# Optimization experiments

Hardware: AMD Instinct MI355X
Metric: run time of the kernel (lower is better)

The kernel has to match this reference:

```python
import jax, jax.numpy as jnp
import numpy as np

S, B, C = 7, 2, 80
LAMBDA_COORDS = 5.0
LAMBDA_NOOBJ = 0.5


def _iou_cxcywh(a, b):
    """Elementwise IoU of boxes in cx,cy,w,h format, shapes (..., 4) -> (...).
    Same math as torchvision box_convert(cxcywh->xyxy) + box_iou diagonal,
    computed directly (O(S^2)) instead of the O(S^4) pairwise matrix."""
    ax1 = a[..., 0] - a[..., 2] * 0.5
    ay1 = a[..., 1] - a[..., 3] * 0.5
    ax2 = a[..., 0] + a[..., 2] * 0.5
    ay2 = a[..., 1] + a[..., 3] * 0.5
    bx1 = b[..., 0] - b[..., 2] * 0.5
    by1 = b[..., 1] - b[..., 3] * 0.5
    bx2 = b[..., 0] + b[..., 2] * 0.5
    by2 = b[..., 1] + b[..., 3] * 0.5
    inter_w = jnp.clip(jnp.minimum(ax2, bx2) - jnp.maximum(ax1, bx1), 0.0)
    inter_h = jnp.clip(jnp.minimum(ay2, by2) - jnp.maximum(ay1, by1), 0.0)
    inter = inter_w * inter_h
    area_a = (ax2 - ax1) * (ay2 - ay1)
    area_b = (bx2 - bx1) * (by2 - by1)
    return inter / (area_a + area_b - inter)


def setup_inputs() -> dict:
    key = jax.random.key(0)
    k1, k2 = jax.random.split(key)
    N = 8192
    predictions = jax.random.normal(k1, (N, S, S, C + 5 * B), dtype=jnp.float32)
    target = jax.random.uniform(k2, (N, S, S, C + 5), dtype=jnp.float32)
    return {"predictions": predictions, "target": target}


def reference(predictions, target):
    preds = predictions.reshape(-1, S, S, C + 5 * B)
    target_boxes = target[..., -4:]                 # (N,S,S,4)
    pred_boxes_1 = preds[..., -4:]
    pred_boxes_2 = preds[..., -9:-5]

    iou1 = _iou_cxcywh(pred_boxes_1, target_boxes)  # (N,S,S) == diag of box_iou
    iou2 = _iou_cxcywh(pred_boxes_2, target_boxes)
    ious_idx = jnp.argmax(jnp.stack([iou1, iou2], axis=0), axis=0)  # (N,S,S)

    m1 = (1 - ious_idx).astype(preds.dtype)  # responsible-box masks
    m2 = ious_idx.astype(preds.dtype)
    obj = target[..., -5]                    # objectness (N,S,S)

    pred_boxes = obj[..., None] * (m1[..., None] * pred_boxes_1 + m2[..., None] * pred_boxes_2)

    dims = jnp.sign(pred_boxes[..., -2:]) * jnp.sqrt(jnp.abs(pred_boxes[..., -2:]) + 1e-6)
    target_dims = jnp.sqrt(target_boxes[..., -2:])

    sse = lambda a, b: jnp.sum((a - b) ** 2)  # MSELoss(reduction='sum')

    center_loss = sse(pred_boxes[..., :-3], target_boxes[..., :-3]) * LAMBDA_COORDS
    dimensions_loss = sse(dims, target_dims) * LAMBDA_COORDS
    coords_loss = center_loss + dimensions_loss

    obj_pred = preds[..., -5] * m1 + preds[..., -10] * m2
    obj_loss = sse(obj * obj_pred, obj)
    noobj_loss = sse((1.0 - obj) * obj_pred, obj) * LAMBDA_NOOBJ

    classes_loss = sse(preds[..., :-10] * obj[..., None], target[..., :-5])

    return (coords_loss, obj_loss, noobj_loss, classes_loss)
```

## Files before the change

kernel.cpp:

```cpp
#include <hip/hip_runtime.h>


#define NPRED 90
#define NTGT  85
#define NCLS  80

__device__ __forceinline__ float sgnf(float x) {
    return (x > 0.0f) ? 1.0f : ((x < 0.0f) ? -1.0f : 0.0f);
}

__device__ __forceinline__ float iou_vs_target(
    float acx, float acy, float aw, float ah,
    float bx1, float by1, float bx2, float by2, float area_b)
{
    float ax1 = acx - aw * 0.5f, ay1 = acy - ah * 0.5f;
    float ax2 = acx + aw * 0.5f, ay2 = acy + ah * 0.5f;
    float iw = fmaxf(fminf(ax2, bx2) - fmaxf(ax1, bx1), 0.0f);
    float ih = fmaxf(fminf(ay2, by2) - fmaxf(ay1, by1), 0.0f);
    float inter = iw * ih;
    float area_a = (ax2 - ax1) * (ay2 - ay1);
    return inter / (area_a + area_b - inter);
}

__global__ __launch_bounds__(256) void yolo_loss_kernel(
    const float* __restrict__ preds, const float* __restrict__ targ,
    float* __restrict__ out, int n_cells)
{
    float coords = 0.0f, objl = 0.0f, noobjl = 0.0f, clsl = 0.0f;

    int tid    = blockIdx.x * 256 + threadIdx.x;
    int stride = gridDim.x * 256;

    for (int cell = tid; cell < n_cells; cell += stride) {
        const float* p = preds + (size_t)cell * NPRED;
        const float* t = targ  + (size_t)cell * NTGT;
        const float2* p2 = (const float2*)p;

        float obj = t[NCLS];

        float cls = 0.0f;
        #pragma unroll 10
        for (int k = 0; k < NCLS / 2; ++k) {
            float2 pv = p2[k];
            float d0 = fmaf(pv.x, obj, -t[2 * k]);
            float d1 = fmaf(pv.y, obj, -t[2 * k + 1]);
            cls = fmaf(d0, d0, cls);
            cls = fmaf(d1, d1, cls);
        }
        clsl += cls;

        float2 q0 = p2[40];
        float2 q1 = p2[41];
        float2 q2 = p2[42];
        float2 q3 = p2[43];
        float2 q4 = p2[44];

        float tcx = t[81], tcy = t[82], tw = t[83], th = t[84];
        float bx1 = tcx - tw * 0.5f, by1 = tcy - th * 0.5f;
        float bx2 = tcx + tw * 0.5f, by2 = tcy + th * 0.5f;
        float area_b = (bx2 - bx1) * (by2 - by1);

        float iou1 = iou_vs_target(q3.x, q3.y, q4.x, q4.y, bx1, by1, bx2, by2, area_b);
        float iou2 = iou_vs_target(q0.y, q1.x, q1.y, q2.x, bx1, by1, bx2, by2, area_b);
        bool use2 = iou2 > iou1;

        float pcx = obj * (use2 ? q0.y : q3.x);
        float pw  = obj * (use2 ? q1.y : q4.x);
        float ph  = obj * (use2 ? q2.x : q4.y);

        float dc = pcx - tcx;
        float dw = sgnf(pw) * sqrtf(fabsf(pw) + 1e-6f) - sqrtf(tw);
        float dh = sgnf(ph) * sqrtf(fabsf(ph) + 1e-6f) - sqrtf(th);
        coords = fmaf(dc, dc, coords);
        coords = fmaf(dw, dw, coords);
        coords = fmaf(dh, dh, coords);

        float obj_pred = use2 ? q0.x : q2.y;
        float e1 = fmaf(obj, obj_pred, -obj);
        objl = fmaf(e1, e1, objl);
        float e2 = fmaf(1.0f - obj, obj_pred, -obj);
        noobjl = fmaf(e2, e2, noobjl);
    }

    #pragma unroll
    for (int off = 32; off > 0; off >>= 1) {
        coords += __shfl_down(coords, off);
        objl   += __shfl_down(objl, off);
        noobjl += __shfl_down(noobjl, off);
        clsl   += __shfl_down(clsl, off);
    }

    __shared__ float red[4][4];
    int wave = threadIdx.x >> 6;
    int lane = threadIdx.x & 63;
    if (lane == 0) {
        red[0][wave] = coords;
        red[1][wave] = objl;
        red[2][wave] = noobjl;
        red[3][wave] = clsl;
    }
    __syncthreads();
    if (threadIdx.x == 0) {
        float c = red[0][0] + red[0][1] + red[0][2] + red[0][3];
        float o = red[1][0] + red[1][1] + red[1][2] + red[1][3];
        float n = red[2][0] + red[2][1] + red[2][2] + red[2][3];
        float k = red[3][0] + red[3][1] + red[3][2] + red[3][3];
        atomicAdd(&out[0], 5.0f * c);
        atomicAdd(&out[1], o);
        atomicAdd(&out[2], 0.5f * n);
        atomicAdd(&out[3], k);
    }
}

extern "C" void kernel_launch(void* const* d_in, const int* in_sizes, int n_in,
                              void* d_out, int out_size, void* d_ws, size_t ws_size,
                              hipStream_t stream) {
    const float* preds = (const float*)d_in[0];
    const float* targ  = (const float*)d_in[1];
    float* out = (float*)d_out;

    int n_cells = in_sizes[0] / NPRED;

    hipMemsetAsync(d_out, 0, (size_t)out_size * sizeof(float), stream);

    int blocks = (n_cells + 255) / 256;
    hipLaunchKernelGGL(yolo_loss_kernel, dim3(blocks), dim3(256), 0, stream,
                       preds, targ, out, n_cells);
}
```

Before: 333.3 us.

## Stage cell chunks through LDS with coalesced float4 loads

Instead of each thread reading one cell's 90+85 floats with strided accesses, each block loads a chunk of 64 cells with fully coalesced float4 loads, staging targets in shared memory and streaming prediction quads directly. Class loss is computed per quad with lookups into LDS targets, and box components are scattered to a small LDS buffer so 64 threads can compute the IoU and coordinate losses. This is meant to fix the uncoalesced per-thread strided global access pattern, at the cost of extra syncthreads, LDS traffic, per-element branching, and only a quarter of threads doing the box work.

```diff
diff --git a/kernel.cpp b/kernel.cpp
--- a/kernel.cpp
+++ b/kernel.cpp
@@ -4,6 +4,12 @@
 #define NPRED 90
 #define NTGT  85
 #define NCLS  80
+#define CHUNK 64
+#define TPB   256
+#define PBS   11
+
+#define NT4 (CHUNK * NTGT / 4)
+#define NP4 (CHUNK * NPRED / 4)
 
 __device__ __forceinline__ float sgnf(float x) {
     return (x > 0.0f) ? 1.0f : ((x < 0.0f) ? -1.0f : 0.0f);
@@ -22,60 +28,152 @@
     return inter / (area_a + area_b - inter);
 }
 
-__global__ __launch_bounds__(256) void yolo_loss_kernel(
+__device__ __forceinline__ void proc_elem(float v, int cl, int j,
+    const float* __restrict__ t_lds, float* __restrict__ pbox, float& clsl)
+{
+    if (j < NCLS) {
+        float obj = t_lds[cl * NTGT + NCLS];
+        float tv  = t_lds[cl * NTGT + j];
+        float d = fmaf(v, obj, -tv);
+        clsl = fmaf(d, d, clsl);
+    } else {
+        pbox[cl * PBS + (j - NCLS)] = v;
+    }
+}
+
+__device__ __forceinline__ void proc_quad(float4 v, int q,
+    const float* __restrict__ t_lds, float* __restrict__ pbox, float& clsl)
+{
+    int f  = 4 * q;
+    int cl = f / NPRED;
+    int j  = f - cl * NPRED;
+    proc_elem(v.x, cl, j, t_lds, pbox, clsl); ++j;
+    proc_elem(v.y, cl, j, t_lds, pbox, clsl); ++j;
+    if (j == NPRED) { j = 0; ++cl; }
+    proc_elem(v.z, cl, j, t_lds, pbox, clsl); ++j;
+    proc_elem(v.w, cl, j, t_lds, pbox, clsl);
+}
+
+__global__ __launch_bounds__(TPB) void yolo_loss_kernel(
     const float* __restrict__ preds, const float* __restrict__ targ,
     float* __restrict__ out, int n_cells)
 {
+    __shared__ __align__(16) float t_lds[CHUNK * NTGT];
+    __shared__ float pbox[CHUNK * PBS];
+    __shared__ float red[4][4];
+
     float coords = 0.0f, objl = 0.0f, noobjl = 0.0f, clsl = 0.0f;
 
-    int tid    = blockIdx.x * 256 + threadIdx.x;
-    int stride = gridDim.x * 256;
-
-    for (int cell = tid; cell < n_cells; cell += stride) {
+    const int tid = threadIdx.x;
+    const int n_chunks = n_cells / CHUNK;
+
+    for (int ch = blockIdx.x; ch < n_chunks; ch += gridDim.x) {
+        const float4* tg4 = (const float4*)(targ  + (size_t)ch * (CHUNK * NTGT));
+        const float4* pr4 = (const float4*)(preds + (size_t)ch * (CHUNK * NPRED));
+
+        float4 t0 = tg4[tid];
+        float4 t1 = tg4[tid + 256];
+        float4 t2 = tg4[tid + 512];
+        float4 t3 = tg4[tid + 768];
+        float4 t4 = tg4[tid + 1024];
+        const bool ht = tid < (NT4 - 1280);
+        float4 t5 = make_float4(0.f, 0.f, 0.f, 0.f);
+        if (ht) t5 = tg4[tid + 1280];
+
+        float4 p0 = pr4[tid];
+        float4 p1 = pr4[tid + 256];
+        float4 p2 = pr4[tid + 512];
+        float4 p3 = pr4[tid + 768];
+        float4 p4 = pr4[tid + 1024];
+        const bool hp = tid < (NP4 - 1280);
+        float4 p5 = make_float4(0.f, 0.f, 0.f, 0.f);
+        if (hp) p5 = pr4[tid + 1280];
+
+        __syncthreads();
+
+        float4* tl4 = (float4*)t_lds;
+        tl4[tid]        = t0;
+        tl4[tid + 256]  = t1;
+        tl4[tid + 512]  = t2;
+        tl4[tid + 768]  = t3;
+        tl4[tid + 1024] = t4;
+        if (ht) tl4[tid + 1280] = t5;
+
+        __syncthreads();
+
+        proc_quad(p0, tid,        t_lds, pbox, clsl);
+        proc_quad(p1, tid + 256,  t_lds, pbox, clsl);
+        proc_quad(p2, tid + 512,  t_lds, pbox, clsl);
+        proc_quad(p3, tid + 768,  t_lds, pbox, clsl);
+        proc_quad(p4, tid + 1024, t_lds, pbox, clsl);
+        if (hp) proc_quad(p5, tid + 1280, t_lds, pbox, clsl);
+
+        __syncthreads();
+
+        if (tid < CHUNK) {
+            const float* pb = &pbox[tid * PBS];
+            const float* tc = &t_lds[tid * NTGT + NCLS];
+            float obj = tc[0];
+            float tcx = tc[1], tcy = tc[2], tw = tc[3], th = tc[4];
+            float bx1 = tcx - tw * 0.5f, by1 = tcy - th * 0.5f;
+            float bx2 = tcx + tw * 0.5f, by2 = tcy + th * 0.5f;
+            float area_b = (bx2 - bx1) * (by2 - by1);
+
+            float iou1 = iou_vs_target(pb[6], pb[7], pb[8], pb[9],
+                                       bx1, by1, bx2, by2, area_b);
+            float iou2 = iou_vs_target(pb[1], pb[2], pb[3], pb[4],
+                                       bx1, by1, bx2, by2, area_b);
+            bool use2 = iou2 > iou1;
+
+            float pcx = obj * (use2 ? pb[1] : pb[6]);
+            float pw  = obj * (use2 ? pb[3] : pb[8]);
+            float ph  = obj * (use2 ? pb[4] : pb[9]);
+
+            float dc = pcx - tcx;
+            float dw = sgnf(pw) * sqrtf(fabsf(pw) + 1e-6f) - sqrtf(tw);
+            float dh = sgnf(ph) * sqrtf(fabsf(ph) + 1e-6f) - sqrtf(th);
+            coords = fmaf(dc, dc, coords);
+            coords = fmaf(dw, dw, coords);
+            coords = fmaf(dh, dh, coords);
+
+            float obj_pred = use2 ? pb[0] : pb[5];
+            float e1 = fmaf(obj, obj_pred, -obj);
+            objl = fmaf(e1, e1, objl);
+            float e2 = fmaf(1.0f - obj, obj_pred, -obj);
+            noobjl = fmaf(e2, e2, noobjl);
+        }
+    }
+
+    for (int cell = n_chunks * CHUNK + (int)(blockIdx.x * TPB + tid);
+         cell < n_cells; cell += gridDim.x * TPB) {
         const float* p = preds + (size_t)cell * NPRED;
         const float* t = targ  + (size_t)cell * NTGT;
-        const float2* p2 = (const float2*)p;
-
         float obj = t[NCLS];
-
         float cls = 0.0f;
-        #pragma unroll 10
-        for (int k = 0; k < NCLS / 2; ++k) {
-            float2 pv = p2[k];
-            float d0 = fmaf(pv.x, obj, -t[2 * k]);
-            float d1 = fmaf(pv.y, obj, -t[2 * k + 1]);
-            cls = fmaf(d0, d0, cls);
-            cls = fmaf(d1, d1, cls);
+        for (int k = 0; k < NCLS; ++k) {
+            float d = fmaf(p[k], obj, -t[k]);
+            cls = fmaf(d, d, cls);
         }
         clsl += cls;
-
-        float2 q0 = p2[40];
-        float2 q1 = p2[41];
-        float2 q2 = p2[42];
-        float2 q3 = p2[43];
-        float2 q4 = p2[44];
-
         float tcx = t[81], tcy = t[82], tw = t[83], th = t[84];
         float bx1 = tcx - tw * 0.5f, by1 = tcy - th * 0.5f;
         float bx2 = tcx + tw * 0.5f, by2 = tcy + th * 0.5f;
         float area_b = (bx2 - bx1) * (by2 - by1);
-
-        float iou1 = iou_vs_target(q3.x, q3.y, q4.x, q4.y, bx1, by1, bx2, by2, area_b);
-        float iou2 = iou_vs_target(q0.y, q1.x, q1.y, q2.x, bx1, by1, bx2, by2, area_b);
+        float iou1 = iou_vs_target(p[86], p[87], p[88], p[89],
+                                   bx1, by1, bx2, by2, area_b);
+        float iou2 = iou_vs_target(p[81], p[82], p[83], p[84],
+                                   bx1, by1, bx2, by2, area_b);
         bool use2 = iou2 > iou1;
-
-        float pcx = obj * (use2 ? q0.y : q3.x);
-        float pw  = obj * (use2 ? q1.y : q4.x);
-        float ph  = obj * (use2 ? q2.x : q4.y);
-
+        float pcx = obj * (use2 ? p[81] : p[86]);
+        float pw  = obj * (use2 ? p[83] : p[88]);
+        float ph  = obj * (use2 ? p[84] : p[89]);
         float dc = pcx - tcx;
         float dw = sgnf(pw) * sqrtf(fabsf(pw) + 1e-6f) - sqrtf(tw);
         float dh = sgnf(ph) * sqrtf(fabsf(ph) + 1e-6f) - sqrtf(th);
         coords = fmaf(dc, dc, coords);
         coords = fmaf(dw, dw, coords);
         coords = fmaf(dh, dh, coords);
-
-        float obj_pred = use2 ? q0.x : q2.y;
+        float obj_pred = use2 ? p[80] : p[85];
         float e1 = fmaf(obj, obj_pred, -obj);
         objl = fmaf(e1, e1, objl);
         float e2 = fmaf(1.0f - obj, obj_pred, -obj);
@@ -90,9 +188,9 @@
         clsl   += __shfl_down(clsl, off);
     }
 
-    __shared__ float red[4][4];
     int wave = threadIdx.x >> 6;
     int lane = threadIdx.x & 63;
+    __syncthreads();
     if (lane == 0) {
         red[0][wave] = coords;
         red[1][wave] = objl;
@@ -120,10 +218,11 @@
     float* out = (float*)d_out;
 
     int n_cells = in_sizes[0] / NPRED;
+    int n_chunks = n_cells / CHUNK;
 
     hipMemsetAsync(d_out, 0, (size_t)out_size * sizeof(float), stream);
 
-    int blocks = (n_cells + 255) / 256;
-    hipLaunchKernelGGL(yolo_loss_kernel, dim3(blocks), dim3(256), 0, stream,
+    int blocks = n_chunks > 0 ? n_chunks : 1;
+    hipLaunchKernelGGL(yolo_loss_kernel, dim3(blocks), dim3(TPB), 0, stream,
                        preds, targ, out, n_cells);
 }
```

Result: slower. 520.6 us (+56.2%).

## Coalesce class-loss reads via flat float4 stream and two-stage block reduction

Applied to the files above, without the earlier changes.

Replaces the per-cell strided walk over 90-float prediction rows with a flat, fully coalesced float4 stream over the whole predictions buffer. Each quad works out its cell and offset by integer division and reads the matching target entries. Box and objectness terms are handled in a second per-cell loop over a fixed grid of 2048 blocks. Per-block partial sums now go to a workspace and a small second kernel reduces them, replacing the memset and global atomics. The costs are extra index arithmetic, branching on quads that straddle cell boundaries, scattered target reads, and a second pass over the box fields.

```diff
diff --git a/kernel.cpp b/kernel.cpp
--- a/kernel.cpp
+++ b/kernel.cpp
@@ -1,9 +1,12 @@
 #include <hip/hip_runtime.h>
+#include <stdint.h>
 
 
 #define NPRED 90
 #define NTGT  85
 #define NCLS  80
+#define TPB   256
+#define NBLK  2048
 
 __device__ __forceinline__ float sgnf(float x) {
     return (x > 0.0f) ? 1.0f : ((x < 0.0f) ? -1.0f : 0.0f);
@@ -22,51 +25,89 @@
     return inter / (area_a + area_b - inter);
 }
 
-__global__ __launch_bounds__(256) void yolo_loss_kernel(
+__device__ __forceinline__ void class_quad(
+    const float4* __restrict__ pr4, const float* __restrict__ targ,
+    long long q, float& clsl)
+{
+    float4 v = pr4[q];
+    unsigned f  = (unsigned)(4ll * q);
+    unsigned cl = f / 90u;
+    unsigned j  = f - cl * 90u;
+    const float* tb = targ + (size_t)cl * NTGT;
+    if (j <= 76u) {
+        float obj = tb[NCLS];
+        float d0 = fmaf(v.x, obj, -tb[j]);
+        float d1 = fmaf(v.y, obj, -tb[j + 1]);
+        float d2 = fmaf(v.z, obj, -tb[j + 2]);
+        float d3 = fmaf(v.w, obj, -tb[j + 3]);
+        clsl = fmaf(d0, d0, clsl);
+        clsl = fmaf(d1, d1, clsl);
+        clsl = fmaf(d2, d2, clsl);
+        clsl = fmaf(d3, d3, clsl);
+    } else if (j == 78u) {
+        float obj = tb[NCLS];
+        float d0 = fmaf(v.x, obj, -tb[78]);
+        float d1 = fmaf(v.y, obj, -tb[79]);
+        clsl = fmaf(d0, d0, clsl);
+        clsl = fmaf(d1, d1, clsl);
+    } else if (j == 88u) {
+        const float* t2 = tb + NTGT;
+        float obj2 = t2[NCLS];
+        float d0 = fmaf(v.z, obj2, -t2[0]);
+        float d1 = fmaf(v.w, obj2, -t2[1]);
+        clsl = fmaf(d0, d0, clsl);
+        clsl = fmaf(d1, d1, clsl);
+    }
+}
+
+__global__ __launch_bounds__(TPB, 2) void yolo_loss_kernel(
     const float* __restrict__ preds, const float* __restrict__ targ,
-    float* __restrict__ out, int n_cells)
-{
+    float* __restrict__ part, float* __restrict__ out,
+    int n_cells, int mode)
+{
+    __shared__ float red[4][4];
+
     float coords = 0.0f, objl = 0.0f, noobjl = 0.0f, clsl = 0.0f;
 
-    int tid    = blockIdx.x * 256 + threadIdx.x;
-    int stride = gridDim.x * 256;
-
-    for (int cell = tid; cell < n_cells; cell += stride) {
-        const float* p = preds + (size_t)cell * NPRED;
-        const float* t = targ  + (size_t)cell * NTGT;
-        const float2* p2 = (const float2*)p;
-
-        float obj = t[NCLS];
-
-        float cls = 0.0f;
-        #pragma unroll 10
-        for (int k = 0; k < NCLS / 2; ++k) {
-            float2 pv = p2[k];
-            float d0 = fmaf(pv.x, obj, -t[2 * k]);
-            float d1 = fmaf(pv.y, obj, -t[2 * k + 1]);
-            cls = fmaf(d0, d0, cls);
-            cls = fmaf(d1, d1, cls);
-        }
-        clsl += cls;
-
-        float2 q0 = p2[40];
-        float2 q1 = p2[41];
-        float2 q2 = p2[42];
-        float2 q3 = p2[43];
-        float2 q4 = p2[44];
-
-        float tcx = t[81], tcy = t[82], tw = t[83], th = t[84];
+    const int tid = threadIdx.x;
+    const long long tid0    = (long long)blockIdx.x * TPB + tid;
+    const long long tstride = (long long)gridDim.x * TPB;
+
+    const long long n_quads = ((long long)n_cells * NPRED) / 4;
+    const float4* pr4 = (const float4*)preds;
+
+    long long q = tid0;
+    for (; q + tstride < n_quads; q += 2 * tstride) {
+        class_quad(pr4, targ, q,           clsl);
+        class_quad(pr4, targ, q + tstride, clsl);
+    }
+    for (; q < n_quads; q += tstride)
+        class_quad(pr4, targ, q, clsl);
+
+    for (long long c = tid0; c < n_cells; c += tstride) {
+        const float* pB = preds + (size_t)c * NPRED + NCLS;
+        const float* tB = targ  + (size_t)c * NTGT + NCLS;
+        float2 b0 = *(const float2*)(pB);
+        float2 b1 = *(const float2*)(pB + 2);
+        float2 b2 = *(const float2*)(pB + 4);
+        float2 b3 = *(const float2*)(pB + 6);
+        float2 b4 = *(const float2*)(pB + 8);
+        float obj = tB[0];
+        float tcx = tB[1], tcy = tB[2], tw = tB[3], th = tB[4];
+
         float bx1 = tcx - tw * 0.5f, by1 = tcy - th * 0.5f;
         float bx2 = tcx + tw * 0.5f, by2 = tcy + th * 0.5f;
         float area_b = (bx2 - bx1) * (by2 - by1);
 
-        float iou1 = iou_vs_target(q3.x, q3.y, q4.x, q4.y, bx1, by1, bx2, by2, area_b);
-        float iou2 = iou_vs_target(q0.y, q1.x, q1.y, q2.x, bx1, by1, bx2, by2, area_b);
+        float iou1 = iou_vs_target(b3.x, b3.y, b4.x, b4.y,
+                                   bx1, by1, bx2, by2, area_b);
+        float iou2 = iou_vs_target(b0.y, b1.x, b1.y, b2.x,
+                                   bx1, by1, bx2, by2, area_b);
         bool use2 = iou2 > iou1;
 
-        float pcx = obj * (use2 ? q0.y : q3.x);
-        float pw  = obj * (use2 ? q1.y : q4.x);
-        float ph  = obj * (use2 ? q2.x : q4.y);
+        float pcx = obj * (use2 ? b0.y : b3.x);
+        float pw  = obj * (use2 ? b1.y : b4.x);
+        float ph  = obj * (use2 ? b2.x : b4.y);
 
         float dc = pcx - tcx;
         float dw = sgnf(pw) * sqrtf(fabsf(pw) + 1e-6f) - sqrtf(tw);
@@ -75,7 +116,7 @@
         coords = fmaf(dw, dw, coords);
         coords = fmaf(dh, dh, coords);
 
-        float obj_pred = use2 ? q0.x : q2.y;
+        float obj_pred = use2 ? b0.x : b2.y;
         float e1 = fmaf(obj, obj_pred, -obj);
         objl = fmaf(e1, e1, objl);
         float e2 = fmaf(1.0f - obj, obj_pred, -obj);
@@ -90,9 +131,8 @@
         clsl   += __shfl_down(clsl, off);
     }
 
-    __shared__ float red[4][4];
-    int wave = threadIdx.x >> 6;
-    int lane = threadIdx.x & 63;
+    int wave = tid >> 6;
+    int lane = tid & 63;
     if (lane == 0) {
         red[0][wave] = coords;
         red[1][wave] = objl;
@@ -100,15 +140,38 @@
         red[3][wave] = clsl;
     }
     __syncthreads();
-    if (threadIdx.x == 0) {
+    if (tid == 0) {
         float c = red[0][0] + red[0][1] + red[0][2] + red[0][3];
         float o = red[1][0] + red[1][1] + red[1][2] + red[1][3];
         float n = red[2][0] + red[2][1] + red[2][2] + red[2][3];
         float k = red[3][0] + red[3][1] + red[3][2] + red[3][3];
-        atomicAdd(&out[0], 5.0f * c);
-        atomicAdd(&out[1], o);
-        atomicAdd(&out[2], 0.5f * n);
-        atomicAdd(&out[3], k);
+        if (mode == 0) {
+            int nb = gridDim.x;
+            part[0 * nb + blockIdx.x] = c;
+            part[1 * nb + blockIdx.x] = o;
+            part[2 * nb + blockIdx.x] = n;
+            part[3 * nb + blockIdx.x] = k;
+        } else {
+            atomicAdd(&out[0], 5.0f * c);
+            atomicAdd(&out[1], o);
+            atomicAdd(&out[2], 0.5f * n);
+            atomicAdd(&out[3], k);
+        }
+    }
+}
+
+__global__ __launch_bounds__(256) void yolo_reduce_kernel(
+    const float* __restrict__ part, float* __restrict__ out, int nblk)
+{
+    int w = threadIdx.x >> 6;
+    int lane = threadIdx.x & 63;
+    float s = 0.0f;
+    for (int i = lane; i < nblk; i += 64) s += part[w * nblk + i];
+    #pragma unroll
+    for (int off = 32; off > 0; off >>= 1) s += __shfl_down(s, off);
+    if (lane == 0) {
+        float scale = (w == 0) ? 5.0f : (w == 2) ? 0.5f : 1.0f;
+        out[w] = s * scale;
     }
 }
 
@@ -121,9 +184,20 @@
 
     int n_cells = in_sizes[0] / NPRED;
 
-    hipMemsetAsync(d_out, 0, (size_t)out_size * sizeof(float), stream);
-
-    int blocks = (n_cells + 255) / 256;
-    hipLaunchKernelGGL(yolo_loss_kernel, dim3(blocks), dim3(256), 0, stream,
-                       preds, targ, out, n_cells);
-}
+    bool use_ws = ws_size >= (size_t)(4 * NBLK) * sizeof(float);
+
+    if (use_ws) {
+        float* part = (float*)d_ws;
+        hipLaunchKernelGGL(yolo_loss_kernel, dim3(NBLK), dim3(TPB), 0, stream,
+                           preds, targ, part, out, n_cells, 0);
+        hipLaunchKernelGGL(yolo_reduce_kernel, dim3(1), dim3(256), 0, stream,
+                           part, out, NBLK);
+        if (out_size > 4) {
+            hipMemsetAsync(out + 4, 0, (size_t)(out_size - 4) * sizeof(float), stream);
+        }
+    } else {
+        hipMemsetAsync(d_out, 0, (size_t)out_size * sizeof(float), stream);
+        hipLaunchKernelGGL(yolo_loss_kernel, dim3(NBLK), dim3(TPB), 0, stream,
+                           preds, targ, (float*)nullptr, out, n_cells, 1);
+    }
+}
```

Result: faster. 309.0 us (-7.3%).
